# Kernel optimization log

Measured on AMD Instinct MI355X. Metric: run time of the kernel, lower is better.

## Reference

```python
import jax, jax.numpy as jnp
import numpy as np

# fixed 9 neighborhood offsets (center + 8 directions), in pixel units
BASE = np.array([[0,0],[-1,-1],[0,-1],[1,-1],[-1,0],[1,0],[-1,1],[0,1],[1,1]], dtype=np.float32)
MAX_DELTA = 0.5 / 512.0


def bilinear_sample(vm, gx, gy):
    """vm: (D,H,W); gx,gy: (N,) normalized grid coords in [-1,1].
    Bilinear, padding_mode='zeros', align_corners=True. Returns (D,N)."""
    D, H, W = vm.shape
    ix = (gx + 1.0) * 0.5 * (W - 1)
    iy = (gy + 1.0) * 0.5 * (H - 1)
    x0 = jnp.floor(ix); y0 = jnp.floor(iy)
    x1 = x0 + 1.0;      y1 = y0 + 1.0
    wx1 = ix - x0; wx0 = 1.0 - wx1
    wy1 = iy - y0; wy0 = 1.0 - wy1
    fm = vm.reshape(D, H * W)

    def corner(xf, yf, wx, wy):
        valid = (xf >= 0) & (xf <= W - 1) & (yf >= 0) & (yf <= H - 1)
        xi = jnp.clip(xf.astype(jnp.int32), 0, W - 1)
        yi = jnp.clip(yf.astype(jnp.int32), 0, H - 1)
        v = jnp.take(fm, yi * W + xi, axis=1)  # (D,N) gather
        w = jnp.where(valid, wx * wy, 0.0)
        return v * w

    return (corner(x0, y0, wx0, wy0) + corner(x1, y0, wx1, wy0)
            + corner(x0, y1, wx0, wy1) + corner(x1, y1, wx1, wy1))


def setup_inputs() -> dict:
    key = jax.random.key(0)
    ks = jax.random.split(key, 5)
    B, C, Hf, Wf = 4, 256, 128, 128
    T, D = 16384, 128
    fmap = jax.random.normal(ks[0], (B, C, Hf, Wf), dtype=jnp.float32)
    coords = jax.random.uniform(ks[1], (B, T, 2), dtype=jnp.float32)
    W_proj = jax.random.normal(ks[2], (D, C), dtype=jnp.float32) * (1.0 / np.sqrt(C))
    W1 = jax.random.normal(ks[3], (D, D), dtype=jnp.float32) * (1.0 / np.sqrt(D))
    b1 = jnp.zeros((D,), dtype=jnp.float32)
    W2 = jax.random.normal(ks[4], (2, D), dtype=jnp.float32) * (1.0 / np.sqrt(D))
    b2 = jnp.zeros((2,), dtype=jnp.float32)
    return {"fmap": fmap, "coords": coords, "W_proj": W_proj,
            "W1": W1, "b1": b1, "W2": W2, "b2": b2}


def reference(fmap, coords, W_proj, W1, b1, W2, b2):
    B, C, Hf, Wf = fmap.shape
    T = coords.shape[1]
    K = BASE.shape[0]
    # 1x1 conv projection
    vm = jnp.einsum('bchw,dc->bdhw', fmap, W_proj)  # (B,D,Hf,Wf)
    # offsets: one pixel step in [0,1] coords (align_corners=True)
    step = jnp.array([1.0 / (Wf - 1), 1.0 / (Hf - 1)], dtype=coords.dtype)
    grid = coords[:, :, None, :] + jnp.asarray(BASE)[None, None] * step  # (B,T,K,2)
    grid = grid * 2.0 - 1.0                                            # normalize to [-1,1]
    grid = grid.reshape(B, T * K, 2)
    feat = jax.vmap(bilinear_sample)(vm, grid[..., 0], grid[..., 1])   # (B,D,T*K)
    D = feat.shape[1]
    feat = feat.transpose(0, 2, 1).reshape(B, T, K, D).mean(axis=2)    # (B,T,D)
    h = jax.nn.relu(feat @ W1.T + b1)
    delta = jnp.tanh(h @ W2.T + b2) * MAX_DELTA
    return coords + delta
```

## Files before the change

### kernel.cpp

```cpp
#include <hip/hip_runtime.h>
#include <cstddef>

#define NB 4
#define NC 256
#define ND 128
#define NH 128
#define NW 128
#define NHW (NH*NW)
#define NT 16384
#define NBKT 1024
#define CAP 192

typedef short   short8  __attribute__((ext_vector_type(8)));
typedef float   floatx4 __attribute__((ext_vector_type(4)));
typedef float   floatx2 __attribute__((ext_vector_type(2)));

__device__ __forceinline__ unsigned pk_bf16(float a, float b) {
    unsigned ua = __float_as_uint(a);
    unsigned ub = __float_as_uint(b);
    ua += 0x7fffu + ((ua >> 16) & 1u);
    ub += 0x7fffu + ((ub >> 16) & 1u);
    return (ua >> 16) | (ub & 0xffff0000u);
}

__device__ __forceinline__ unsigned fp8x4_from_f32(float v0, float v1, float v2, float v3) {
    int r = 0;
    r = __builtin_amdgcn_cvt_pk_fp8_f32(v0, v1, r, false);
    r = __builtin_amdgcn_cvt_pk_fp8_f32(v2, v3, r, true);
    return (unsigned)r;
}
template <bool HI>
__device__ __forceinline__ floatx2 fp8x2_to_f32(unsigned w) {
    return __builtin_amdgcn_cvt_pk_f32_fp8((int)w, HI);
}

__device__ __forceinline__ int bucket_of(float cx, float cy, int b) {
    int x0 = (int)floorf(cx * (float)(NW - 1));
    int y0 = (int)floorf(cy * (float)(NH - 1));
    x0 = min(max(x0, 0), NW - 1);
    y0 = min(max(y0, 0), NH - 1);
    return b * 256 + (y0 >> 3) * 16 + (x0 >> 3);
}

__global__ __launch_bounds__(256)
void prep_kernel(const float* __restrict__ W1, const float* __restrict__ Wp,
                 unsigned short* __restrict__ Wfbf, int* __restrict__ counts)
{
    const int bi = blockIdx.x;
    const int t  = threadIdx.x;
    if (bi == 16) {
        counts[t*4+0] = 0; counts[t*4+1] = 0; counts[t*4+2] = 0; counts[t*4+3] = 0;
        return;
    }
    const int e  = bi*8 + (t >> 5);
    const int c0 = (t & 31) * 8;
    float acc[8];
    #pragma unroll
    for (int j = 0; j < 8; ++j) acc[j] = 0.f;
    const float* w1r = W1 + (size_t)e*ND;
    const float* wpc = Wp + c0;
    for (int d = 0; d < ND; ++d) {
        const float s = w1r[d];
        float4 p0 = *(const float4*)(wpc + (size_t)d*NC);
        float4 p1 = *(const float4*)(wpc + (size_t)d*NC + 4);
        acc[0] = fmaf(s, p0.x, acc[0]); acc[1] = fmaf(s, p0.y, acc[1]);
        acc[2] = fmaf(s, p0.z, acc[2]); acc[3] = fmaf(s, p0.w, acc[3]);
        acc[4] = fmaf(s, p1.x, acc[4]); acc[5] = fmaf(s, p1.y, acc[5]);
        acc[6] = fmaf(s, p1.z, acc[6]); acc[7] = fmaf(s, p1.w, acc[7]);
    }
    uint4 pk = make_uint4(pk_bf16(acc[0],acc[1]), pk_bf16(acc[2],acc[3]),
                          pk_bf16(acc[4],acc[5]), pk_bf16(acc[6],acc[7]));
    *(uint4*)&Wfbf[(size_t)e*NC + c0] = pk;
}

__global__ __launch_bounds__(512, 4)
void proj_fill_kernel(const float* __restrict__ fmap,
                      const unsigned short* __restrict__ Wfbf,
                      const float* __restrict__ coords,
                      unsigned char* __restrict__ vmf,
                      int* __restrict__ counts, int* __restrict__ order)
{
    const int bi0 = blockIdx.x;
    if (bi0 < 128) {
        const int g = bi0 * 512 + threadIdx.x;
        const float cx = coords[(size_t)g*2 + 0];
        const float cy = coords[(size_t)g*2 + 1];
        const int bkt = bucket_of(cx, cy, g >> 14);
        const int pos = atomicAdd(&counts[bkt], 1);
        if (pos < CAP) order[bkt*CAP + pos] = g;
        return;
    }
    const int bi = bi0 - 128;
    __shared__ unsigned short awp[4*8*64*8];

    const int t    = threadIdx.x;
    const int lane = t & 63;
    const int w    = t >> 6;
    const int l15  = lane & 15;
    const int q    = lane >> 4;
    const int cq   = q * 8;

    const int h    = bi & 1;
    const int bi2  = bi >> 1;
    const int b    = (bi2 & 7) >> 1;
    const int slot = ((bi2 >> 3) << 1) | (bi2 & 1);
    const int p    = slot*128 + w*16 + l15;

    {
        const int dt  = w >> 1;
        const int ch0 = (w & 1) * 4;
        #pragma unroll
        for (int cc = 0; cc < 4; ++cc) {
            const int ch = ch0 + cc;
            uint4 v = *(const uint4*)&Wfbf[(size_t)(h*64 + dt*16 + l15)*NC + ch*32 + cq];
            *(uint4*)&awp[((dt*8 + ch)*64 + lane)*8] = v;
        }
    }
    __syncthreads();

    floatx4 acc[4];
    #pragma unroll
    for (int i = 0; i < 4; ++i) acc[i] = (floatx4)(0.f);

    const float* fbase = fmap + (size_t)b*NC*NHW + p;

    float f[64];
    #pragma unroll
    for (int c0 = 0; c0 < 8; ++c0)
        #pragma unroll
        for (int j = 0; j < 8; ++j)
            f[c0*8 + j] = fbase[(size_t)(c0*32 + cq + j)*NHW];

    #pragma unroll
    for (int c0 = 0; c0 < 8; ++c0) {
        union { short8 v; unsigned u[4]; } bc;
        #pragma unroll
        for (int j = 0; j < 4; ++j) bc.u[j] = pk_bf16(f[c0*8 + 2*j], f[c0*8 + 2*j+1]);
        #pragma unroll
        for (int dt = 0; dt < 4; ++dt) {
            short8 afr = *(const short8*)&awp[((dt*8 + c0)*64 + lane)*8];
            acc[dt] = __builtin_amdgcn_mfma_f32_16x16x32_bf16(afr, bc.v, acc[dt], 0, 0, 0);
        }
    }
    unsigned char* vrow = vmf + ((size_t)(b*NHW + p))*ND + h*64;
    #pragma unroll
    for (int dt = 0; dt < 4; ++dt) {
        floatx4 v = acc[dt];
        *(unsigned*)&vrow[dt*16 + q*4] = fp8x4_from_f32(v[0], v[1], v[2], v[3]);
    }
}

__global__ __launch_bounds__(512, 4)
void gather_kernel(const unsigned char* __restrict__ vmf, const float* __restrict__ coords,
                   const int* __restrict__ counts, const int* __restrict__ order,
                   const float* __restrict__ b1, const float* __restrict__ W2,
                   const float* __restrict__ b2, float* __restrict__ out)
{
    const int t   = threadIdx.x;
    const int bkt = blockIdx.x;
    const int n   = min(counts[bkt], CAP);
    const int grp = t >> 3;
    const int c8  = t & 7;
    const int e0  = c8 * 16;
    const float b20 = b2[0], b21 = b2[1];
    const float MD = 0.5f / 512.0f;
    const float s9 = 1.f / 9.f;

    for (int i = grp; i < n; i += 64) {
        const int g = order[bkt*CAP + i];
        const int b = g >> 14;
        const float cx = coords[(size_t)g*2 + 0];
        const float cy = coords[(size_t)g*2 + 1];
        const float ix = cx * (float)(NW - 1);
        const float iy = cy * (float)(NH - 1);
        const float x0f = floorf(ix), y0f = floorf(iy);
        const int x0 = (int)x0f, y0 = (int)y0f;
        const float wx1 = ix - x0f, wy1 = iy - y0f;
        const float wxv[4] = {1.f - wx1, 1.f, 1.f, wx1};
        const float wyv[4] = {1.f - wy1, 1.f, 1.f, wy1};
        floatx2 acc[8];
        #pragma unroll
        for (int k = 0; k < 8; ++k) acc[k] = (floatx2)(0.f);
        const unsigned char* vmb = vmf + (size_t)b*NHW*ND + e0;
        #pragma unroll
        for (int j = 0; j < 4; ++j) {
            const int Y  = y0 - 1 + j;
            const int Yc = min(max(Y, 0), NH-1);
            const bool vy = (Y >= 0) & (Y < NH);
            #pragma unroll
            for (int ii = 0; ii < 4; ++ii) {
                const int X  = x0 - 1 + ii;
                const int Xc = min(max(X, 0), NW-1);
                const bool vx = (X >= 0) & (X < NW);
                const float wgt = (vx & vy) ? wxv[ii]*wyv[j] : 0.f;
                uint4 u = *(const uint4*)(vmb + (size_t)(Yc*NW + Xc)*ND);
                const floatx2 w2v = {wgt, wgt};
                acc[0] += w2v * fp8x2_to_f32<false>(u.x);
                acc[1] += w2v * fp8x2_to_f32<true >(u.x);
                acc[2] += w2v * fp8x2_to_f32<false>(u.y);
                acc[3] += w2v * fp8x2_to_f32<true >(u.y);
                acc[4] += w2v * fp8x2_to_f32<false>(u.z);
                acc[5] += w2v * fp8x2_to_f32<true >(u.z);
                acc[6] += w2v * fp8x2_to_f32<false>(u.w);
                acc[7] += w2v * fp8x2_to_f32<true >(u.w);
            }
        }
        float s0 = 0.f, s1 = 0.f;
        #pragma unroll
        for (int k = 0; k < 8; ++k) {
            float2 bb = *(const float2*)&b1[e0 + 2*k];
            float h0 = fmaxf(fmaf(acc[k].x, s9, bb.x), 0.f);
            float h1 = fmaxf(fmaf(acc[k].y, s9, bb.y), 0.f);
            float2 wa = *(const float2*)&W2[e0 + 2*k];
            float2 wb = *(const float2*)&W2[ND + e0 + 2*k];
            s0 = fmaf(h0, wa.x, fmaf(h1, wa.y, s0));
            s1 = fmaf(h0, wb.x, fmaf(h1, wb.y, s1));
        }
        s0 += __shfl_xor(s0, 1); s0 += __shfl_xor(s0, 2); s0 += __shfl_xor(s0, 4);
        s1 += __shfl_xor(s1, 1); s1 += __shfl_xor(s1, 2); s1 += __shfl_xor(s1, 4);
        if (c8 == 0) {
            float2 o = make_float2(cx + tanhf(s0 + b20) * MD,
                                   cy + tanhf(s1 + b21) * MD);
            *(float2*)&out[(size_t)g*2] = o;
        }
    }
}

extern "C" void kernel_launch(void* const* d_in, const int* in_sizes, int n_in,
                              void* d_out, int out_size, void* d_ws, size_t ws_size,
                              hipStream_t stream)
{
    const float* fmap   = (const float*)d_in[0];
    const float* coords = (const float*)d_in[1];
    const float* Wp     = (const float*)d_in[2];
    const float* W1     = (const float*)d_in[3];
    const float* b1     = (const float*)d_in[4];
    const float* W2     = (const float*)d_in[5];
    const float* b2     = (const float*)d_in[6];
    float* out = (float*)d_out;

    unsigned char* vmf = (unsigned char*)d_ws;
    char* base = (char*)d_ws + (size_t)NB*NHW*ND;
    unsigned short* Wfbf = (unsigned short*)base;
    int* counts = (int*)(base + 65536);
    int* order  = (int*)(base + 65536 + 4096);

    prep_kernel     <<<dim3(17),         256, 0, stream>>>(W1, Wp, Wfbf, counts);
    proj_fill_kernel<<<dim3(128 + 1024), 512, 0, stream>>>(fmap, Wfbf, coords,
                                                           vmf, counts, order);
    gather_kernel   <<<dim3(NBKT),       512, 0, stream>>>(vmf, coords, counts, order,
                                                           b1, W2, b2, out);
}
```

Measured before the change: 159.6 us.

## Stage fmap tiles into LDS with double-buffered async global-to-LDS loads

The projection kernel used to load 64 strided fmap values per thread straight into registers before any MFMA work. It now stages 32-channel by 128-pixel tiles in shared memory using 16-byte global_load_lds copies, double-buffered so the next channel chunk loads while the current one feeds the MFMAs. It also remaps block indices so blocks that share fmap data run closer together. This is meant to get wide, coalesced row loads, lower register pressure and overlap of loads with compute. In exchange it adds 32 KB of LDS and a barrier in every channel iteration.

```diff
diff --git a/kernel.cpp b/kernel.cpp
--- a/kernel.cpp
+++ b/kernel.cpp
@@ -32,6 +32,12 @@
 template <bool HI>
 __device__ __forceinline__ floatx2 fp8x2_to_f32(unsigned w) {
     return __builtin_amdgcn_cvt_pk_f32_fp8((int)w, HI);
+}
+
+__device__ __forceinline__ void async16(const float* g, float* l) {
+    __builtin_amdgcn_global_load_lds(
+        (const __attribute__((address_space(1))) unsigned int*)g,
+        (__attribute__((address_space(3))) unsigned int*)l, 16, 0, 0);
 }
 
 __device__ __forceinline__ int bucket_of(float cx, float cy, int b) {
@@ -91,6 +97,7 @@
         return;
     }
     const int bi = bi0 - 128;
+    __shared__ float stage[2][32*128];
     __shared__ unsigned short awp[4*8*64*8];
 
     const int t    = threadIdx.x;
@@ -100,11 +107,13 @@
     const int q    = lane >> 4;
     const int cq   = q * 8;
 
-    const int h    = bi & 1;
-    const int bi2  = bi >> 1;
-    const int b    = (bi2 & 7) >> 1;
-    const int slot = ((bi2 >> 3) << 1) | (bi2 & 1);
-    const int p    = slot*128 + w*16 + l15;
+    const int x    = bi & 7;
+    const int m    = bi >> 3;
+    const int h    = m & 1;
+    const int slot = ((x & 1) << 6) | (m >> 1);
+    const int b    = x >> 1;
+    const int p0   = slot * 128;
+    const int p    = p0 + w*16 + l15;
 
     {
         const int dt  = w >> 1;
@@ -116,31 +125,42 @@
             *(uint4*)&awp[((dt*8 + ch)*64 + lane)*8] = v;
         }
     }
+
+    const float* fb = fmap + (size_t)b*NC*NHW + p0 + (lane & 31)*4;
+    const int cw = w*4 + (lane >> 5);
+
+    #pragma unroll
+    for (int i = 0; i < 2; ++i)
+        async16(fb + (size_t)(cw + i*2)*NHW, &stage[0][(w*4 + i*2)*128]);
+
     __syncthreads();
 
     floatx4 acc[4];
     #pragma unroll
     for (int i = 0; i < 4; ++i) acc[i] = (floatx4)(0.f);
 
-    const float* fbase = fmap + (size_t)b*NC*NHW + p;
-
-    float f[64];
-    #pragma unroll
-    for (int c0 = 0; c0 < 8; ++c0)
+    #pragma unroll
+    for (int c0 = 0; c0 < 8; ++c0) {
+        const int s = c0 & 1;
+        if (c0 < 7) {
+            #pragma unroll
+            for (int i = 0; i < 2; ++i)
+                async16(fb + (size_t)((c0+1)*32 + cw + i*2)*NHW,
+                        &stage[s^1][(w*4 + i*2)*128]);
+        }
+        float f[8];
         #pragma unroll
         for (int j = 0; j < 8; ++j)
-            f[c0*8 + j] = fbase[(size_t)(c0*32 + cq + j)*NHW];
-
-    #pragma unroll
-    for (int c0 = 0; c0 < 8; ++c0) {
+            f[j] = stage[s][(cq + j)*128 + w*16 + l15];
         union { short8 v; unsigned u[4]; } bc;
         #pragma unroll
-        for (int j = 0; j < 4; ++j) bc.u[j] = pk_bf16(f[c0*8 + 2*j], f[c0*8 + 2*j+1]);
+        for (int j = 0; j < 4; ++j) bc.u[j] = pk_bf16(f[2*j], f[2*j+1]);
         #pragma unroll
         for (int dt = 0; dt < 4; ++dt) {
             short8 afr = *(const short8*)&awp[((dt*8 + c0)*64 + lane)*8];
             acc[dt] = __builtin_amdgcn_mfma_f32_16x16x32_bf16(afr, bc.v, acc[dt], 0, 0, 0);
         }
+        __syncthreads();
     }
     unsigned char* vrow = vmf + ((size_t)(b*NHW + p))*ND + h*64;
     #pragma unroll
```

Measured after the change: 157.4 us. Within noise of the previous version (-1.4%).
